# Performance work log

Hardware: AMD Instinct MI355X
Metric: run time of the kernel (lower is better)

The kernel has to match this reference:

```python
import jax, jax.numpy as jnp
import numpy as np

N = 50000; E = 800000; F_IN = 165; HID = 32; H1 = 8; H3 = 4; OUT = 2
D1 = H1 * HID  # 256
D3 = H3 * HID  # 128
BN_EPS = 1e-5


def _gat_conv(x, edge_index, W, a_s, a_d, b, heads, add_self_loops):
    n = x.shape[0]
    if add_self_loops:
        loops = jnp.arange(n, dtype=edge_index.dtype)
        edge_index = jnp.concatenate([edge_index, jnp.stack([loops, loops])], axis=1)
    src, dst = edge_index[0], edge_index[1]
    h = (x @ W).reshape(n, heads, -1)                      # [N, H, D]
    a_src = jnp.sum(h * a_s, axis=-1)                      # [N, H]
    a_dst = jnp.sum(h * a_d, axis=-1)                      # [N, H]
    e = jax.nn.leaky_relu(a_src[src] + a_dst[dst], 0.2)    # [E, H] per-edge logits
    m = jax.ops.segment_max(e, dst, num_segments=n)        # segment-softmax over incoming edges
    ex = jnp.exp(e - m[dst])
    den = jax.ops.segment_sum(ex, dst, num_segments=n)
    alpha = ex / (den[dst] + 1e-16)                        # PyG softmax eps
    out = jax.ops.segment_sum(h[src] * alpha[:, :, None], dst, num_segments=n)
    return out.reshape(n, -1) + b                          # concat heads + bias


def _bn(x, g, b, mean, var):  # eval-mode BatchNorm1d
    return (x - mean) * jax.lax.rsqrt(var + BN_EPS) * g + b


def setup_inputs() -> dict:
    key = jax.random.key(0)
    ks = jax.random.split(key, 24)
    rn = lambda i, shape, s=0.05: jax.random.normal(ks[i], shape, dtype=jnp.float32) * s
    d = {}
    d["x"] = jax.random.normal(ks[0], (N, F_IN), dtype=jnp.float32)
    d["edge_index"] = jax.random.randint(ks[1], (2, E), 0, N, dtype=jnp.int32)
    d["W1"] = rn(2, (F_IN, D1)); d["a1s"] = rn(3, (H1, HID)); d["a1d"] = rn(4, (H1, HID))
    d["b1"] = jnp.zeros((D1,), jnp.float32)
    d["g1"] = jnp.ones((D1,), jnp.float32); d["be1"] = jnp.zeros((D1,), jnp.float32)
    d["m1"] = rn(5, (D1,)); d["v1"] = jax.random.uniform(ks[6], (D1,), minval=0.5, maxval=1.5)
    d["W2"] = rn(7, (D1, D1)); d["a2s"] = rn(8, (H1, HID)); d["a2d"] = rn(9, (H1, HID))
    d["b2"] = jnp.zeros((D1,), jnp.float32)
    d["g2"] = jnp.ones((D1,), jnp.float32); d["be2"] = jnp.zeros((D1,), jnp.float32)
    d["m2"] = rn(10, (D1,)); d["v2"] = jax.random.uniform(ks[11], (D1,), minval=0.5, maxval=1.5)
    d["W3"] = rn(12, (D1, D3)); d["a3s"] = rn(13, (H3, HID)); d["a3d"] = rn(14, (H3, HID))
    d["b3"] = jnp.zeros((D3,), jnp.float32)
    d["fcW"] = rn(15, (D3, OUT)); d["fcb"] = jnp.zeros((OUT,), jnp.float32)
    d["skW"] = rn(16, (F_IN, D3)); d["skb"] = jnp.zeros((D3,), jnp.float32)
    d["temp"] = jnp.array(1.0, jnp.float32)
    return d


def reference(x, edge_index, W1, a1s, a1d, b1, g1, be1, m1, v1,
              W2, a2s, a2d, b2, g2, be2, m2, v2,
              W3, a3s, a3d, b3, fcW, fcb, skW, skb, temp):
    x_init = x @ skW + skb                                   # skip Linear
    h = jax.nn.elu(_bn(_gat_conv(x, edge_index, W1, a1s, a1d, b1, H1, False), g1, be1, m1, v1))
    h = jax.nn.elu(_bn(_gat_conv(h, edge_index, W2, a2s, a2d, b2, H1, True), g2, be2, m2, v2) + h)
    h = _gat_conv(h * temp, edge_index, W3, a3s, a3d, b3, H3, True)
    return jax.nn.log_softmax((h + x_init) @ fcW + fcb, axis=1)
```

## Files before the change

kernel.cpp:

```cpp
#include <hip/hip_runtime.h>
#include <hip/hip_bf16.h>
#include <math.h>

#define N_NODES 50000
#define MP      50048
#define N_EDGES 800000
#define F_IN    165
#define KPAD1   192
#define D1      256
#define D3      128
#define CAP     64

typedef __attribute__((ext_vector_type(8))) short short8;
typedef __attribute__((ext_vector_type(4))) float floatx4;
typedef __attribute__((ext_vector_type(2))) float floatx2;

__device__ __forceinline__ float bflo(unsigned u) { return __uint_as_float(u << 16); }
__device__ __forceinline__ float bfhi(unsigned u) { return __uint_as_float(u & 0xffff0000u); }

__device__ __forceinline__ void fma8p(floatx2* a, float wgt, const uint4& v) {
    floatx2 w2; w2.x = wgt; w2.y = wgt;
    floatx2 p;
    p.x = bflo(v.x); p.y = bfhi(v.x); a[0] += w2 * p;
    p.x = bflo(v.y); p.y = bfhi(v.y); a[1] += w2 * p;
    p.x = bflo(v.z); p.y = bfhi(v.z); a[2] += w2 * p;
    p.x = bflo(v.w); p.y = bfhi(v.w); a[3] += w2 * p;
}

#if defined(__has_builtin)
#if __has_builtin(__builtin_amdgcn_global_load_lds)
#define HAS_GLL 1
#endif
#endif

__device__ __forceinline__ void gload16(const void* g, void* lds) {
#ifdef HAS_GLL
    __builtin_amdgcn_global_load_lds(
        (const __attribute__((address_space(1))) unsigned*)g,
        (__attribute__((address_space(3))) unsigned*)lds, 16, 0, 0);
#else
    *(int4*)lds = *(const int4*)g;
#endif
}

__global__ void prep_all(const float* __restrict__ x, __hip_bfloat16* __restrict__ xb,
                         const float* __restrict__ W1, __hip_bfloat16* __restrict__ Wt1,
                         const float* __restrict__ skW, __hip_bfloat16* __restrict__ skWt,
                         const float* __restrict__ W2, __hip_bfloat16* __restrict__ Wt2,
                         const float* __restrict__ W3, __hip_bfloat16* __restrict__ Wt3)
{
    const long long S0 = (long long)MP * KPAD1;
    const long long S1 = S0 + D1 * KPAD1;
    const long long S2 = S1 + D3 * KPAD1;
    const long long S3 = S2 + D1 * D1;
    const long long S4 = S3 + D3 * D1;
    long long idx = (long long)blockIdx.x * 256 + threadIdx.x;
    if (idx < S0) {
        const int m = idx / KPAD1, k = idx - (long long)m * KPAD1;
        xb[idx] = __float2bfloat16((k < F_IN && m < N_NODES) ? x[(size_t)m * F_IN + k] : 0.f);
    } else if (idx < S1) {
        const long long i = idx - S0;
        const int n = i / KPAD1, k = i - (long long)n * KPAD1;
        Wt1[i] = __float2bfloat16((k < F_IN) ? W1[(size_t)k * D1 + n] : 0.f);
    } else if (idx < S2) {
        const long long i = idx - S1;
        const int n = i / KPAD1, k = i - (long long)n * KPAD1;
        skWt[i] = __float2bfloat16((k < F_IN) ? skW[(size_t)k * D3 + n] : 0.f);
    } else if (idx < S3) {
        const long long i = idx - S2;
        const int n = i / D1, k = i - (long long)n * D1;
        Wt2[i] = __float2bfloat16(W2[(size_t)k * D1 + n]);
    } else if (idx < S4) {
        const long long i = idx - S3;
        const int n = i / D1, k = i - (long long)n * D1;
        Wt3[i] = __float2bfloat16(W3[(size_t)k * D3 + n]);
    }
}

__global__ __launch_bounds__(256) void gemm_bf16(
    const __hip_bfloat16* __restrict__ A, const __hip_bfloat16* __restrict__ Bt,
    const float* __restrict__ bias, const float* __restrict__ alphap,
    float* __restrict__ Cf, __hip_bfloat16* __restrict__ Cb, int M, int Ka, int NN)
{
    __shared__ short As[128 * 32];
    __shared__ short Bs[128 * 32];
    const int t  = threadIdx.x;
    const int m0 = blockIdx.x * 128;
    const int n0 = blockIdx.y * 128;
    const int w  = t >> 6, l = t & 63;
    const int wy = w >> 1, wx = w & 1;
    const int lm = l & 15, quad = l >> 4;
    const float alpha = alphap ? alphap[0] : 1.f;

    floatx4 acc[4][4] = {};

    const int ch0 = w * 128 + l;
    const int ch1 = ch0 + 64;
    const int r0a = ch0 >> 2, k0a = (ch0 & 3) * 8;
    const int r1a = ch1 >> 2, k1a = (ch1 & 3) * 8;

    for (int k0 = 0; k0 < Ka; k0 += 32) {
        gload16(A  + (size_t)(m0 + r0a) * Ka + k0 + k0a, &As[ch0 * 8]);
        gload16(A  + (size_t)(m0 + r1a) * Ka + k0 + k1a, &As[ch1 * 8]);
        gload16(Bt + (size_t)(n0 + r0a) * Ka + k0 + k0a, &Bs[ch0 * 8]);
        gload16(Bt + (size_t)(n0 + r1a) * Ka + k0 + k1a, &Bs[ch1 * 8]);
        __syncthreads();

        short8 af[4], bf[4];
#pragma unroll
        for (int i = 0; i < 4; ++i) {
            af[i] = *(const short8*)&As[(wy * 64 + i * 16 + lm) * 32 + quad * 8];
            bf[i] = *(const short8*)&Bs[(wx * 64 + i * 16 + lm) * 32 + quad * 8];
        }
#pragma unroll
        for (int mi = 0; mi < 4; ++mi)
#pragma unroll
            for (int ni = 0; ni < 4; ++ni)
                acc[mi][ni] = __builtin_amdgcn_mfma_f32_16x16x32_bf16(
                    af[mi], bf[ni], acc[mi][ni], 0, 0, 0);
        __syncthreads();
    }

#pragma unroll
    for (int mi = 0; mi < 4; ++mi) {
#pragma unroll
        for (int r = 0; r < 4; ++r) {
            const int gm = m0 + wy * 64 + mi * 16 + quad * 4 + r;
            if (gm >= M) continue;
#pragma unroll
            for (int ni = 0; ni < 4; ++ni) {
                const int gn = n0 + wx * 64 + ni * 16 + lm;
                float v = acc[mi][ni][r] * alpha;
                if (bias) v += bias[gn];
                if (Cf) Cf[(size_t)gm * NN + gn] = v;
                if (Cb) Cb[(size_t)gm * NN + gn] = __float2bfloat16(v);
            }
        }
    }
}

__global__ void attn_prep(const __hip_bfloat16* __restrict__ h, const float* __restrict__ a_s,
                          const float* __restrict__ a_d, float* __restrict__ osrc,
                          float* __restrict__ odst, int Nn, int hshift)
{
    const int H   = 1 << hshift;
    const int gid = blockIdx.x * blockDim.x + threadIdx.x;
    if (gid >= Nn * H) return;
    const int n  = gid >> hshift;
    const int hh = gid & (H - 1);
    const uint4* hp = (const uint4*)(h + (size_t)n * (H * 32) + hh * 32);
    const float* ap = a_s + hh * 32;
    const float* bp = a_d + hh * 32;
    float s1 = 0.f, s2 = 0.f;
#pragma unroll
    for (int c = 0; c < 4; ++c) {
        const uint4 v = hp[c];
        const unsigned uu[4] = {v.x, v.y, v.z, v.w};
#pragma unroll
        for (int j = 0; j < 4; ++j) {
            const int d = c * 8 + j * 2;
            const float e0 = bflo(uu[j]), e1 = bfhi(uu[j]);
            s1 += e0 * ap[d] + e1 * ap[d + 1];
            s2 += e0 * bp[d] + e1 * bp[d + 1];
        }
    }
    osrc[gid] = s1;
    odst[gid] = s2;
}

__global__ void deg_hist(const int* __restrict__ ei, int* __restrict__ deg, int E)
{
    const int e = blockIdx.x * blockDim.x + threadIdx.x;
    if (e < E) atomicAdd(&deg[ei[E + e]], 1);
}

__global__ __launch_bounds__(1024) void scan_rowptr(const int* __restrict__ deg,
                                                    int* __restrict__ rowptr, int n)
{
    __shared__ int sums[1024];
    const int tid = threadIdx.x;
    const int chunk = (n + 1023) / 1024;
    const int lo = tid * chunk;
    const int hi = min(lo + chunk, n);
    int s = 0;
    for (int i = lo; i < hi; ++i) s += deg[i];
    sums[tid] = s;
    __syncthreads();
    for (int off = 1; off < 1024; off <<= 1) {
        int t = 0;
        if (tid >= off) t = sums[tid - off];
        __syncthreads();
        if (tid >= off) sums[tid] += t;
        __syncthreads();
    }
    int run = sums[tid] - s;
    for (int i = lo; i < hi; ++i) { rowptr[i] = run; run += deg[i]; }
    if (lo < n && hi == n) rowptr[n] = run;
}

__global__ void csr_fill(const int* __restrict__ ei, const int* __restrict__ rowptr,
                         int* __restrict__ cursor, int* __restrict__ csr_src, int E)
{
    const int e = blockIdx.x * blockDim.x + threadIdx.x;
    if (e >= E) return;
    const int dst = ei[E + e];
    const int pos = rowptr[dst] + atomicAdd(&cursor[dst], 1);
    csr_src[pos] = ei[e];
}

template <int HSH, int D, int POST>
__global__ __launch_bounds__(256) void gat_gather_v8(
    const __hip_bfloat16* __restrict__ h, const float* __restrict__ asrc,
    const float* __restrict__ adst, const int* __restrict__ rowptr,
    const int* __restrict__ csr_src, int selfloop,
    const float* __restrict__ bias, const float* __restrict__ g,
    const float* __restrict__ be, const float* __restrict__ mean,
    const float* __restrict__ var, const float* __restrict__ resid,
    const float* __restrict__ fcW, const float* __restrict__ fcb,
    float* __restrict__ outF, __hip_bfloat16* __restrict__ outB)
{
    constexpr int H    = 1 << HSH;
    constexpr int LPE  = D / 8;
    constexpr int EPW  = 64 / LPE;
    constexpr int SUBS = 64 >> HSH;
    constexpr int MAXJ = CAP / SUBS;

    const int w = threadIdx.x >> 6, l = threadIdx.x & 63;
    const int node = blockIdx.x * 4 + w;

    __shared__ float sW[4][CAP * H];
    __shared__ int   sSrc[4][CAP];

    const int r0  = rowptr[node];
    const int deg = rowptr[node + 1] - r0;
    const int tot = min(deg + selfloop, CAP);

    const int hh  = l & (H - 1);
    const int sub = l >> HSH;
    const float ad = adst[node * H + hh];

    float ex[MAXJ];
    float sum = 0.f;
    {
        int nj = 0;
        for (int e = sub; e < tot; e += SUBS, ++nj) {
            const int s = (e < deg) ? csr_src[r0 + e] : node;
            if (hh == 0) sSrc[w][e] = s;
            float v = asrc[s * H + hh] + ad;
            v = v > 0.f ? v : 0.2f * v;
            ex[nj] = __expf(v);
            sum += ex[nj];
        }
    }
#pragma unroll
    for (int off = H; off < 64; off <<= 1) sum += __shfl_xor(sum, off);
    const float rs = 1.f / (sum + 1e-16f);
    {
        int nj = 0;
        for (int e = sub; e < tot; e += SUBS, ++nj)
            sW[w][e * H + hh] = ex[nj] * rs;
    }

    const int sw   = l / LPE;
    const int lo   = l % LPE;
    const int dimb = lo * 8;
    const int hh2  = dimb >> 5;
    floatx2 a0[4] = {}, a1[4] = {}, a2[4] = {}, a3[4] = {};

    for (int e = sw; e < tot; e += 4 * EPW) {
        const int e1 = e + EPW, e2 = e + 2 * EPW, e3 = e + 3 * EPW;
        const bool v1 = e1 < tot, v2b = e2 < tot, v3 = e3 < tot;
        const int s0 = sSrc[w][e];
        const int s1 = v1 ? sSrc[w][e1] : node;
        const int s2 = v2b ? sSrc[w][e2] : node;
        const int s3 = v3 ? sSrc[w][e3] : node;
        const float w0 = sW[w][e * H + hh2];
        const float w1 = v1 ? sW[w][e1 * H + hh2] : 0.f;
        const float w2 = v2b ? sW[w][e2 * H + hh2] : 0.f;
        const float w3 = v3 ? sW[w][e3 * H + hh2] : 0.f;
        const uint4 q0 = *(const uint4*)&h[(size_t)s0 * D + dimb];
        const uint4 q1 = *(const uint4*)&h[(size_t)s1 * D + dimb];
        const uint4 q2 = *(const uint4*)&h[(size_t)s2 * D + dimb];
        const uint4 q3 = *(const uint4*)&h[(size_t)s3 * D + dimb];
        fma8p(a0, w0, q0);
        fma8p(a1, w1, q1);
        fma8p(a2, w2, q2);
        fma8p(a3, w3, q3);
    }
    float acc[8];
#pragma unroll
    for (int v = 0; v < 4; ++v) {
        const floatx2 s2v = (a0[v] + a1[v]) + (a2[v] + a3[v]);
        acc[v * 2] = s2v.x; acc[v * 2 + 1] = s2v.y;
    }
#pragma unroll
    for (int off = LPE; off < 64; off <<= 1)
#pragma unroll
        for (int v = 0; v < 8; ++v) acc[v] += __shfl_xor(acc[v], off);

    if (POST == 3) {
        float v0 = 0.f, v1 = 0.f;
        if (l < LPE) {
#pragma unroll
            for (int v = 0; v < 8; ++v) {
                const float val = acc[v] + bias[dimb + v] + resid[(size_t)node * D + dimb + v];
                v0 += val * fcW[(dimb + v) * 2 + 0];
                v1 += val * fcW[(dimb + v) * 2 + 1];
            }
        }
#pragma unroll
        for (int off = 1; off < LPE; off <<= 1) {
            v0 += __shfl_xor(v0, off);
            v1 += __shfl_xor(v1, off);
        }
        if (l == 0) {
            const float l0 = v0 + fcb[0], l1 = v1 + fcb[1];
            const float m2 = fmaxf(l0, l1);
            const float lse = m2 + logf(__expf(l0 - m2) + __expf(l1 - m2));
            outF[node * 2 + 0] = l0 - lse;
            outF[node * 2 + 1] = l1 - lse;
        }
    } else {
        if (l < LPE) {
            float r[8];
            __hip_bfloat16 rb[8];
#pragma unroll
            for (int v = 0; v < 8; ++v) {
                const int f = dimb + v;
                float vv = acc[v] + bias[f];
                vv = (vv - mean[f]) * rsqrtf(var[f] + 1e-5f) * g[f] + be[f];
                if (POST == 2) vv += resid[(size_t)node * D + f];
                vv = vv > 0.f ? vv : (__expf(vv) - 1.f);
                r[v] = vv;
                rb[v] = __float2bfloat16(vv);
            }
            if (POST == 1) {
                *(float4*)&outF[(size_t)node * D + dimb]     = *(float4*)&r[0];
                *(float4*)&outF[(size_t)node * D + dimb + 4] = *(float4*)&r[4];
            }
            *(uint4*)&outB[(size_t)node * D + dimb] = *(uint4*)&rb[0];
        }
    }
}

extern "C" void kernel_launch(void* const* d_in, const int* in_sizes, int n_in,
                              void* d_out, int out_size, void* d_ws, size_t ws_size,
                              hipStream_t stream)
{
    const float* x    = (const float*)d_in[0];
    const int*   ei   = (const int*)  d_in[1];
    const float* W1   = (const float*)d_in[2];
    const float* a1s  = (const float*)d_in[3];
    const float* a1d  = (const float*)d_in[4];
    const float* b1   = (const float*)d_in[5];
    const float* g1   = (const float*)d_in[6];
    const float* be1  = (const float*)d_in[7];
    const float* m1   = (const float*)d_in[8];
    const float* v1   = (const float*)d_in[9];
    const float* W2   = (const float*)d_in[10];
    const float* a2s  = (const float*)d_in[11];
    const float* a2d  = (const float*)d_in[12];
    const float* b2   = (const float*)d_in[13];
    const float* g2   = (const float*)d_in[14];
    const float* be2  = (const float*)d_in[15];
    const float* m2   = (const float*)d_in[16];
    const float* v2   = (const float*)d_in[17];
    const float* W3   = (const float*)d_in[18];
    const float* a3s  = (const float*)d_in[19];
    const float* a3d  = (const float*)d_in[20];
    const float* b3   = (const float*)d_in[21];
    const float* fcW  = (const float*)d_in[22];
    const float* fcb  = (const float*)d_in[23];
    const float* skW  = (const float*)d_in[24];
    const float* skb  = (const float*)d_in[25];
    const float* temp = (const float*)d_in[26];

    float* out = (float*)d_out;

    const int N = N_NODES, E = N_EDGES;

    float* ws = (float*)d_ws;
    size_t o = 0;
    float* xinit = ws + o;  o += (size_t)N * D3;
    float* bufC  = ws + o;  o += (size_t)N * D1;
    float* asrc  = ws + o;  o += (size_t)N * 8;
    float* adst  = ws + o;  o += (size_t)N * 8;
    int* rowptr  = (int*)(ws + o);  o += N + 1;
    o = (o + 3) & ~(size_t)3;
    int* csr_src = (int*)(ws + o);  o += E;
    o = (o + 3) & ~(size_t)3;
    __hip_bfloat16* xb    = (__hip_bfloat16*)(ws + o); o += (size_t)MP * KPAD1 / 2;
    __hip_bfloat16* bufCb = (__hip_bfloat16*)(ws + o); o += (size_t)MP * D1 / 2;
    __hip_bfloat16* hb    = (__hip_bfloat16*)(ws + o); o += (size_t)N * D1 / 2;
    __hip_bfloat16* Wt1   = (__hip_bfloat16*)(ws + o); o += (size_t)D1 * KPAD1 / 2;
    __hip_bfloat16* skWt  = (__hip_bfloat16*)(ws + o); o += (size_t)D3 * KPAD1 / 2;
    __hip_bfloat16* Wt2   = (__hip_bfloat16*)(ws + o); o += (size_t)D1 * D1 / 2;
    __hip_bfloat16* Wt3   = (__hip_bfloat16*)(ws + o); o += (size_t)D3 * D1 / 2;
    int* deg    = (int*)bufC;
    int* cursor = deg + N;

    const int MT128 = MP / 128;

    hipMemsetAsync(deg, 0, (size_t)2 * N * sizeof(int), stream);
    deg_hist<<<(E + 255) / 256, 256, 0, stream>>>(ei, deg, E);
    scan_rowptr<<<1, 1024, 0, stream>>>(deg, rowptr, N);
    csr_fill<<<(E + 255) / 256, 256, 0, stream>>>(ei, rowptr, cursor, csr_src, E);

    {
        const long long tote = (long long)MP * KPAD1 + (long long)D1 * KPAD1 +
                               (long long)D3 * KPAD1 + (long long)D1 * D1 + (long long)D3 * D1;
        prep_all<<<(tote + 255) / 256, 256, 0, stream>>>(x, xb, W1, Wt1, skW, skWt, W2, Wt2, W3, Wt3);
    }

    gemm_bf16<<<dim3(MT128, 1), 256, 0, stream>>>(xb, skWt, skb, nullptr, xinit, nullptr, N, KPAD1, D3);

    gemm_bf16<<<dim3(MT128, 2), 256, 0, stream>>>(xb, Wt1, nullptr, nullptr, nullptr, hb, N, KPAD1, D1);
    attn_prep<<<(N * 8 + 255) / 256, 256, 0, stream>>>(hb, a1s, a1d, asrc, adst, N, 3);
    gat_gather_v8<3, D1, 1><<<N / 4, 256, 0, stream>>>(hb, asrc, adst, rowptr, csr_src, 0,
                                                       b1, g1, be1, m1, v1, nullptr, nullptr, nullptr,
                                                       bufC, bufCb);

    gemm_bf16<<<dim3(MT128, 2), 256, 0, stream>>>(bufCb, Wt2, nullptr, nullptr, nullptr, hb, N, D1, D1);
    attn_prep<<<(N * 8 + 255) / 256, 256, 0, stream>>>(hb, a2s, a2d, asrc, adst, N, 3);
    gat_gather_v8<3, D1, 2><<<N / 4, 256, 0, stream>>>(hb, asrc, adst, rowptr, csr_src, 1,
                                                       b2, g2, be2, m2, v2, bufC, nullptr, nullptr,
                                                       nullptr, bufCb);

    gemm_bf16<<<dim3(MT128, 1), 256, 0, stream>>>(bufCb, Wt3, nullptr, temp, nullptr, hb, N, D1, D3);
    attn_prep<<<(N * 4 + 255) / 256, 256, 0, stream>>>(hb, a3s, a3d, asrc, adst, N, 2);
    gat_gather_v8<2, D3, 3><<<N / 4, 256, 0, stream>>>(hb, asrc, adst, rowptr, csr_src, 1,
                                                       b3, nullptr, nullptr, nullptr, nullptr, xinit,
                                                       fcW, fcb, out, nullptr);

    (void)in_sizes; (void)n_in; (void)out_size; (void)ws_size;
}
```

Measured before the change: 650.4 us.

## Fuse skip GEMM into layer-1 GEMM and store residuals in bf16

The skip-connection projection is merged into the first GEMM launch as an extra column tile. Its output goes to a separate bf16 buffer with its own bias. The fp32 copies of the layer-1 output and of the skip projection are dropped, so the residual adds now read bf16 data, which cuts global memory traffic at the cost of some residual precision. The edge-gather loop is also cut from four to two independent accumulators, which lowers register pressure but reduces memory-level parallelism.

```diff
diff --git a/kernel.cpp b/kernel.cpp
--- a/kernel.cpp
+++ b/kernel.cpp
@@ -80,7 +80,8 @@
 __global__ __launch_bounds__(256) void gemm_bf16(
     const __hip_bfloat16* __restrict__ A, const __hip_bfloat16* __restrict__ Bt,
     const float* __restrict__ bias, const float* __restrict__ alphap,
-    float* __restrict__ Cf, __hip_bfloat16* __restrict__ Cb, int M, int Ka, int NN)
+    __hip_bfloat16* __restrict__ Cb, int M, int Ka, int NN, int NNb,
+    __hip_bfloat16* __restrict__ Cx, const float* __restrict__ biasx)
 {
     __shared__ short As[128 * 32];
     __shared__ short Bs[128 * 32];
@@ -131,9 +132,13 @@
             for (int ni = 0; ni < 4; ++ni) {
                 const int gn = n0 + wx * 64 + ni * 16 + lm;
                 float v = acc[mi][ni][r] * alpha;
-                if (bias) v += bias[gn];
-                if (Cf) Cf[(size_t)gm * NN + gn] = v;
-                if (Cb) Cb[(size_t)gm * NN + gn] = __float2bfloat16(v);
+                if (gn < NNb) {
+                    if (bias) v += bias[gn];
+                    Cb[(size_t)gm * NNb + gn] = __float2bfloat16(v);
+                } else {
+                    v += biasx[gn - NNb];
+                    Cx[(size_t)gm * (NN - NNb) + gn - NNb] = __float2bfloat16(v);
+                }
             }
         }
     }
@@ -209,13 +214,13 @@
 }
 
 template <int HSH, int D, int POST>
-__global__ __launch_bounds__(256) void gat_gather_v8(
+__global__ __launch_bounds__(256) void gat_gather_v9(
     const __hip_bfloat16* __restrict__ h, const float* __restrict__ asrc,
     const float* __restrict__ adst, const int* __restrict__ rowptr,
     const int* __restrict__ csr_src, int selfloop,
     const float* __restrict__ bias, const float* __restrict__ g,
     const float* __restrict__ be, const float* __restrict__ mean,
-    const float* __restrict__ var, const float* __restrict__ resid,
+    const float* __restrict__ var, const __hip_bfloat16* __restrict__ residB,
     const float* __restrict__ fcW, const float* __restrict__ fcb,
     float* __restrict__ outF, __hip_bfloat16* __restrict__ outB)
 {
@@ -265,32 +270,24 @@
     const int lo   = l % LPE;
     const int dimb = lo * 8;
     const int hh2  = dimb >> 5;
-    floatx2 a0[4] = {}, a1[4] = {}, a2[4] = {}, a3[4] = {};
-
-    for (int e = sw; e < tot; e += 4 * EPW) {
-        const int e1 = e + EPW, e2 = e + 2 * EPW, e3 = e + 3 * EPW;
-        const bool v1 = e1 < tot, v2b = e2 < tot, v3 = e3 < tot;
-        const int s0 = sSrc[w][e];
-        const int s1 = v1 ? sSrc[w][e1] : node;
-        const int s2 = v2b ? sSrc[w][e2] : node;
-        const int s3 = v3 ? sSrc[w][e3] : node;
-        const float w0 = sW[w][e * H + hh2];
-        const float w1 = v1 ? sW[w][e1 * H + hh2] : 0.f;
-        const float w2 = v2b ? sW[w][e2 * H + hh2] : 0.f;
-        const float w3 = v3 ? sW[w][e3 * H + hh2] : 0.f;
-        const uint4 q0 = *(const uint4*)&h[(size_t)s0 * D + dimb];
-        const uint4 q1 = *(const uint4*)&h[(size_t)s1 * D + dimb];
-        const uint4 q2 = *(const uint4*)&h[(size_t)s2 * D + dimb];
-        const uint4 q3 = *(const uint4*)&h[(size_t)s3 * D + dimb];
-        fma8p(a0, w0, q0);
-        fma8p(a1, w1, q1);
-        fma8p(a2, w2, q2);
-        fma8p(a3, w3, q3);
+    floatx2 a0[4] = {}, a1[4] = {};
+
+    for (int e = sw; e < tot; e += 2 * EPW) {
+        const int e2  = e + EPW;
+        const bool v2 = e2 < tot;
+        const int sa = sSrc[w][e];
+        const int sb = v2 ? sSrc[w][e2] : node;
+        const float wa = sW[w][e * H + hh2];
+        const float wb = v2 ? sW[w][e2 * H + hh2] : 0.f;
+        const uint4 qa = *(const uint4*)&h[(size_t)sa * D + dimb];
+        const uint4 qb = *(const uint4*)&h[(size_t)sb * D + dimb];
+        fma8p(a0, wa, qa);
+        fma8p(a1, wb, qb);
     }
     float acc[8];
 #pragma unroll
     for (int v = 0; v < 4; ++v) {
-        const floatx2 s2v = (a0[v] + a1[v]) + (a2[v] + a3[v]);
+        const floatx2 s2v = a0[v] + a1[v];
         acc[v * 2] = s2v.x; acc[v * 2 + 1] = s2v.y;
     }
 #pragma unroll
@@ -301,9 +298,12 @@
     if (POST == 3) {
         float v0 = 0.f, v1 = 0.f;
         if (l < LPE) {
+            const uint4 rv = *(const uint4*)&residB[(size_t)node * D + dimb];
+            const float rr[8] = {bflo(rv.x), bfhi(rv.x), bflo(rv.y), bfhi(rv.y),
+                                 bflo(rv.z), bfhi(rv.z), bflo(rv.w), bfhi(rv.w)};
 #pragma unroll
             for (int v = 0; v < 8; ++v) {
-                const float val = acc[v] + bias[dimb + v] + resid[(size_t)node * D + dimb + v];
+                const float val = acc[v] + bias[dimb + v] + rr[v];
                 v0 += val * fcW[(dimb + v) * 2 + 0];
                 v1 += val * fcW[(dimb + v) * 2 + 1];
             }
@@ -322,21 +322,23 @@
         }
     } else {
         if (l < LPE) {
-            float r[8];
+            float rr[8] = {};
+            if (POST == 2) {
+                const uint4 rv = *(const uint4*)&residB[(size_t)node * D + dimb];
+                rr[0] = bflo(rv.x); rr[1] = bfhi(rv.x);
+                rr[2] = bflo(rv.y); rr[3] = bfhi(rv.y);
+                rr[4] = bflo(rv.z); rr[5] = bfhi(rv.z);
+                rr[6] = bflo(rv.w); rr[7] = bfhi(rv.w);
+            }
             __hip_bfloat16 rb[8];
 #pragma unroll
             for (int v = 0; v < 8; ++v) {
                 const int f = dimb + v;
                 float vv = acc[v] + bias[f];
                 vv = (vv - mean[f]) * rsqrtf(var[f] + 1e-5f) * g[f] + be[f];
-                if (POST == 2) vv += resid[(size_t)node * D + f];
+                if (POST == 2) vv += rr[v];
                 vv = vv > 0.f ? vv : (__expf(vv) - 1.f);
-                r[v] = vv;
                 rb[v] = __float2bfloat16(vv);
-            }
-            if (POST == 1) {
-                *(float4*)&outF[(size_t)node * D + dimb]     = *(float4*)&r[0];
-                *(float4*)&outF[(size_t)node * D + dimb + 4] = *(float4*)&r[4];
             }
             *(uint4*)&outB[(size_t)node * D + dimb] = *(uint4*)&rb[0];
         }
@@ -381,22 +383,21 @@
 
     float* ws = (float*)d_ws;
     size_t o = 0;
-    float* xinit = ws + o;  o += (size_t)N * D3;
-    float* bufC  = ws + o;  o += (size_t)N * D1;
     float* asrc  = ws + o;  o += (size_t)N * 8;
     float* adst  = ws + o;  o += (size_t)N * 8;
     int* rowptr  = (int*)(ws + o);  o += N + 1;
     o = (o + 3) & ~(size_t)3;
     int* csr_src = (int*)(ws + o);  o += E;
     o = (o + 3) & ~(size_t)3;
-    __hip_bfloat16* xb    = (__hip_bfloat16*)(ws + o); o += (size_t)MP * KPAD1 / 2;
-    __hip_bfloat16* bufCb = (__hip_bfloat16*)(ws + o); o += (size_t)MP * D1 / 2;
-    __hip_bfloat16* hb    = (__hip_bfloat16*)(ws + o); o += (size_t)N * D1 / 2;
-    __hip_bfloat16* Wt1   = (__hip_bfloat16*)(ws + o); o += (size_t)D1 * KPAD1 / 2;
-    __hip_bfloat16* skWt  = (__hip_bfloat16*)(ws + o); o += (size_t)D3 * KPAD1 / 2;
-    __hip_bfloat16* Wt2   = (__hip_bfloat16*)(ws + o); o += (size_t)D1 * D1 / 2;
-    __hip_bfloat16* Wt3   = (__hip_bfloat16*)(ws + o); o += (size_t)D3 * D1 / 2;
-    int* deg    = (int*)bufC;
+    __hip_bfloat16* xb     = (__hip_bfloat16*)(ws + o); o += (size_t)MP * KPAD1 / 2;
+    __hip_bfloat16* bufCb  = (__hip_bfloat16*)(ws + o); o += (size_t)MP * D1 / 2;
+    __hip_bfloat16* hb     = (__hip_bfloat16*)(ws + o); o += (size_t)N * D1 / 2;
+    __hip_bfloat16* xinitB = (__hip_bfloat16*)(ws + o); o += (size_t)N * D3 / 2;
+    __hip_bfloat16* Wt1    = (__hip_bfloat16*)(ws + o); o += (size_t)D1 * KPAD1 / 2;
+    __hip_bfloat16* skWt   = (__hip_bfloat16*)(ws + o); o += (size_t)D3 * KPAD1 / 2;
+    __hip_bfloat16* Wt2    = (__hip_bfloat16*)(ws + o); o += (size_t)D1 * D1 / 2;
+    __hip_bfloat16* Wt3    = (__hip_bfloat16*)(ws + o); o += (size_t)D3 * D1 / 2;
+    int* deg    = (int*)hb;
     int* cursor = deg + N;
 
     const int MT128 = MP / 128;
@@ -412,24 +413,25 @@
         prep_all<<<(tote + 255) / 256, 256, 0, stream>>>(x, xb, W1, Wt1, skW, skWt, W2, Wt2, W3, Wt3);
     }
 
-    gemm_bf16<<<dim3(MT128, 1), 256, 0, stream>>>(xb, skWt, skb, nullptr, xinit, nullptr, N, KPAD1, D3);
-
-    gemm_bf16<<<dim3(MT128, 2), 256, 0, stream>>>(xb, Wt1, nullptr, nullptr, nullptr, hb, N, KPAD1, D1);
+    gemm_bf16<<<dim3(MT128, 3), 256, 0, stream>>>(xb, Wt1, nullptr, nullptr,
+                                                  hb, N, KPAD1, D1 + D3, D1, xinitB, skb);
     attn_prep<<<(N * 8 + 255) / 256, 256, 0, stream>>>(hb, a1s, a1d, asrc, adst, N, 3);
-    gat_gather_v8<3, D1, 1><<<N / 4, 256, 0, stream>>>(hb, asrc, adst, rowptr, csr_src, 0,
+    gat_gather_v9<3, D1, 1><<<N / 4, 256, 0, stream>>>(hb, asrc, adst, rowptr, csr_src, 0,
                                                        b1, g1, be1, m1, v1, nullptr, nullptr, nullptr,
-                                                       bufC, bufCb);
-
-    gemm_bf16<<<dim3(MT128, 2), 256, 0, stream>>>(bufCb, Wt2, nullptr, nullptr, nullptr, hb, N, D1, D1);
+                                                       nullptr, bufCb);
+
+    gemm_bf16<<<dim3(MT128, 2), 256, 0, stream>>>(bufCb, Wt2, nullptr, nullptr,
+                                                  hb, N, D1, D1, D1, nullptr, nullptr);
     attn_prep<<<(N * 8 + 255) / 256, 256, 0, stream>>>(hb, a2s, a2d, asrc, adst, N, 3);
-    gat_gather_v8<3, D1, 2><<<N / 4, 256, 0, stream>>>(hb, asrc, adst, rowptr, csr_src, 1,
-                                                       b2, g2, be2, m2, v2, bufC, nullptr, nullptr,
+    gat_gather_v9<3, D1, 2><<<N / 4, 256, 0, stream>>>(hb, asrc, adst, rowptr, csr_src, 1,
+                                                       b2, g2, be2, m2, v2, bufCb, nullptr, nullptr,
                                                        nullptr, bufCb);
 
-    gemm_bf16<<<dim3(MT128, 1), 256, 0, stream>>>(bufCb, Wt3, nullptr, temp, nullptr, hb, N, D1, D3);
+    gemm_bf16<<<dim3(MT128, 1), 256, 0, stream>>>(bufCb, Wt3, nullptr, temp,
+                                                  hb, N, D1, D3, D3, nullptr, nullptr);
     attn_prep<<<(N * 4 + 255) / 256, 256, 0, stream>>>(hb, a3s, a3d, asrc, adst, N, 2);
-    gat_gather_v8<2, D3, 3><<<N / 4, 256, 0, stream>>>(hb, asrc, adst, rowptr, csr_src, 1,
-                                                       b3, nullptr, nullptr, nullptr, nullptr, xinit,
+    gat_gather_v9<2, D3, 3><<<N / 4, 256, 0, stream>>>(hb, asrc, adst, rowptr, csr_src, 1,
+                                                       b3, nullptr, nullptr, nullptr, nullptr, xinitB,
                                                        fcW, fcb, out, nullptr);
 
     (void)in_sizes; (void)n_in; (void)out_size; (void)ws_size;
```

Measured after the change: 629.4 us. 3.2% less time.
